# Kernel tuning notes

Measured on AMD Instinct MI355X. Metric: run time of the kernel, lower is better.

Reference implementation:

```python
import jax, jax.numpy as jnp
import numpy as np

N_EMBD = 384
HEAD_SIZE = 64
B, T = 512, 256


def setup_inputs() -> dict:
    key = jax.random.key(0)
    ks = jax.random.split(key, 7)
    s = 1.0 / np.sqrt(N_EMBD)  # torch Linear default init scale
    return {
        "x": jax.random.normal(ks[0], (B, T, N_EMBD), dtype=jnp.float32),
        "Wq": jax.random.uniform(ks[1], (N_EMBD, HEAD_SIZE), jnp.float32, -s, s),
        "bq": jax.random.uniform(ks[2], (HEAD_SIZE,), jnp.float32, -s, s),
        "Wk": jax.random.uniform(ks[3], (N_EMBD, HEAD_SIZE), jnp.float32, -s, s),
        "bk": jax.random.uniform(ks[4], (HEAD_SIZE,), jnp.float32, -s, s),
        "Wv": jax.random.uniform(ks[5], (N_EMBD, HEAD_SIZE), jnp.float32, -s, s),
        "bv": jax.random.uniform(ks[6], (HEAD_SIZE,), jnp.float32, -s, s),
    }


def reference(x, Wq, bq, Wk, bk, Wv, bv):
    # Single causal self-attention head (nanoGPT 'Head', eval mode: dropout = identity)
    q = x @ Wq + bq  # [B, T, H]
    k = x @ Wk + bk
    v = x @ Wv + bv
    Tq = x.shape[1]
    scale = x.shape[-1] ** -0.5  # NOTE: source scales by n_embd (C), not head_size
    wei = jnp.einsum("btd,bsd->bts", q, k) * scale  # [B, T, T]
    mask = jnp.tril(jnp.ones((Tq, Tq), dtype=bool))
    wei = jnp.where(mask, wei, -jnp.inf)
    wei = jax.nn.softmax(wei, axis=-1)
    return jnp.einsum("bts,bsd->btd", wei, v)  # [B, T, H]
```

## Files before the change

kernel.cpp:

```cpp
#include <hip/hip_runtime.h>
#include <hip/hip_bf16.h>


#define Bsz 512
#define Tt  256
#define Cc  384
#define Hh  64

typedef __attribute__((ext_vector_type(8))) short bf16x8;
typedef __attribute__((ext_vector_type(4))) float f32x4;

__device__ __forceinline__ unsigned short f2bf(float f) {
    unsigned int u = __float_as_uint(f);
    unsigned int r = (u + 0x7fffu + ((u >> 16) & 1u)) >> 16;
    return (unsigned short)r;
}
__device__ __forceinline__ float bf2f(unsigned short b) {
    return __uint_as_float(((unsigned int)b) << 16);
}
__device__ __forceinline__ bf16x8 pack8(float4 a, float4 b) {
    union { __hip_bfloat162 h2[4]; bf16x8 v; } u;
    u.h2[0] = __float22bfloat162_rn(float2{a.x, a.y});
    u.h2[1] = __float22bfloat162_rn(float2{a.z, a.w});
    u.h2[2] = __float22bfloat162_rn(float2{b.x, b.y});
    u.h2[3] = __float22bfloat162_rn(float2{b.z, b.w});
    return u.v;
}
__device__ __forceinline__ void gload_lds16(const void* g, void* l) {
    __builtin_amdgcn_global_load_lds(
        (const __attribute__((address_space(1))) unsigned int*)g,
        (__attribute__((address_space(3))) unsigned int*)l, 16, 0, 0);
}

__global__ __launch_bounds__(256) void prep_kernel(const float* __restrict__ Wq,
                                                   const float* __restrict__ Wk,
                                                   const float* __restrict__ Wv,
                                                   unsigned short* __restrict__ wtf) {
    int idx = blockIdx.x * 256 + threadIdx.x;
    if (idx >= 192 * 384) return;
    int j = idx & 7;
    int l = (idx >> 3) & 63;
    int t = idx >> 9;
    int kc = t / 12, nt = t - kc * 12;
    int n = nt * 16 + (l & 15);
    int k = kc * 32 + (l >> 4) * 8 + j;
    const float* W = (n < 64) ? Wq : ((n < 128) ? Wk : Wv);
    wtf[idx] = f2bf(W[k * 64 + (n & 63)]);
}

__global__ __launch_bounds__(512, 2) void fused_kernel(
        const float* __restrict__ x,
        const float* __restrict__ bq,
        const float* __restrict__ bk,
        const float* __restrict__ bv,
        const unsigned short* __restrict__ wtf,
        float* __restrict__ out) {
    __shared__ float xl[2][256 * 32];
    __shared__ unsigned short kl[16 * 128 * 8];
    __shared__ unsigned short vl[8 * 4 * 64 * 8];
    __shared__ unsigned short Pl[8 * 512];

    const int tid = threadIdx.x;
    const int w = tid >> 6, lane = tid & 63, quad = lane >> 4, cl = lane & 15;
    const int b = blockIdx.x;
    const int rb = b * 256;

    f32x4 acc[2][12];
#pragma unroll
    for (int rt = 0; rt < 2; ++rt)
#pragma unroll
        for (int nt = 0; nt < 12; ++nt) acc[rt][nt] = (f32x4){0.f, 0.f, 0.f, 0.f};

#pragma unroll
    for (int i = 0; i < 4; ++i) {
        int s = i * 512 + tid;
        int row = s >> 3, cp = s & 7;
        int c = cp ^ (row & 7);
        gload_lds16(x + (size_t)(rb + row) * Cc + c * 4, (char*)xl[0] + (size_t)s * 16);
    }

    for (int kc = 0; kc < 12; ++kc) {
        const int cur = kc & 1;
        bf16x8 bfr[12];
#pragma unroll
        for (int nt = 0; nt < 12; ++nt)
            bfr[nt] = *(const bf16x8*)&wtf[((size_t)(kc * 12 + nt) * 64 + lane) * 8];
        if (kc < 11) {
#pragma unroll
            for (int i = 0; i < 4; ++i) {
                int s = i * 512 + tid;
                int row = s >> 3, cp = s & 7;
                int c = cp ^ (row & 7);
                gload_lds16(x + (size_t)(rb + row) * Cc + (kc + 1) * 32 + c * 4,
                            (char*)xl[cur ^ 1] + (size_t)s * 16);
            }
            asm volatile("s_waitcnt vmcnt(4)" ::: "memory");
        } else {
            asm volatile("s_waitcnt vmcnt(0)" ::: "memory");
        }
        __builtin_amdgcn_s_barrier();

        bf16x8 a[2];
#pragma unroll
        for (int rt = 0; rt < 2; ++rt) {
            int R = w * 32 + rt * 16 + cl;
            float4 lo = *(const float4*)&xl[cur][R * 32 + (((2 * quad) ^ (R & 7)) * 4)];
            float4 hi = *(const float4*)&xl[cur][R * 32 + (((2 * quad + 1) ^ (R & 7)) * 4)];
            a[rt] = pack8(lo, hi);
        }
#pragma unroll
        for (int nt = 0; nt < 12; ++nt) {
            acc[0][nt] = __builtin_amdgcn_mfma_f32_16x16x32_bf16(a[0], bfr[nt], acc[0][nt], 0, 0, 0);
            acc[1][nt] = __builtin_amdgcn_mfma_f32_16x16x32_bf16(a[1], bfr[nt], acc[1][nt], 0, 0, 0);
        }
        __builtin_amdgcn_s_barrier();
    }

    unsigned short* qls = (unsigned short*)xl[0];
#pragma unroll
    for (int nt = 0; nt < 12; ++nt) {
        int col = nt * 16 + cl;
        if (nt < 4) {
            float bias = bq[col];
            int sh = col >> 5, qp = (col >> 3) & 3, j = col & 7;
#pragma unroll
            for (int rt = 0; rt < 2; ++rt) {
                int m0 = w * 32 + rt * 16 + quad * 4;
                int basei = (m0 >> 4) * 1024 + sh * 512 + qp * 128 + quad * 32 + j;
#pragma unroll
                for (int r = 0; r < 4; ++r)
                    qls[basei + r * 8] = f2bf(acc[rt][nt][r] + bias);
            }
        } else if (nt < 8) {
            int h = col & 63;
            float bias = bk[h];
            int sh = h >> 5, qp = (h >> 3) & 3, j = h & 7;
#pragma unroll
            for (int rt = 0; rt < 2; ++rt) {
                int m0 = w * 32 + rt * 16 + quad * 4;
                int basei = (m0 >> 4) * 1024 + sh * 512 + qp * 128 + quad * 32 + j;
#pragma unroll
                for (int r = 0; r < 4; ++r)
                    kl[basei + r * 8] = f2bf(acc[rt][nt][r] + bias);
            }
        } else {
            int h = col - 128;
            float bias = bv[h];
            int ht = h >> 4, clp = h & 15;
#pragma unroll
            for (int rt = 0; rt < 2; ++rt) {
                int m0 = w * 32 + rt * 16 + quad * 4;
                int ks2 = m0 >> 5, qp = (m0 >> 3) & 3, j0 = m0 & 7;
                unsigned long long pk =
                      (unsigned long long)f2bf(acc[rt][nt][0] + bias)
                    | ((unsigned long long)f2bf(acc[rt][nt][1] + bias) << 16)
                    | ((unsigned long long)f2bf(acc[rt][nt][2] + bias) << 32)
                    | ((unsigned long long)f2bf(acc[rt][nt][3] + bias) << 48);
                *(unsigned long long*)&vl[(ks2 * 4 + ht) * 512 + qp * 128 + clp * 8 + j0] = pk;
            }
        }
    }
    __syncthreads();

    const float SL2E = 0.07362224f;
    unsigned short* P = &Pl[w * 512];
#pragma unroll
    for (int ti = 0; ti < 2; ++ti) {
        const int W = ti ? (15 - w) : w;
        const int qrow0 = W * 16;
        bf16x8 aq0 = *(const bf16x8*)&qls[(W * 128 + lane) * 8];
        bf16x8 aq1 = *(const bf16x8*)&qls[(W * 128 + 64 + lane) * 8];

        f32x4 o[4];
#pragma unroll
        for (int ht = 0; ht < 4; ++ht) o[ht] = (f32x4){0.f, 0.f, 0.f, 0.f};
        float rs[4] = {0.f, 0.f, 0.f, 0.f};

        const int nsteps = (qrow0 >> 5) + 1;
        for (int st = 0; st < nsteps; ++st) {
#pragma unroll
            for (int half = 0; half < 2; ++half) {
                int ct = st * 2 + half;
                bf16x8 b0 = *(const bf16x8*)&kl[(ct * 128 + lane) * 8];
                bf16x8 b1 = *(const bf16x8*)&kl[(ct * 128 + 64 + lane) * 8];
                f32x4 sc = (f32x4){0.f, 0.f, 0.f, 0.f};
                sc = __builtin_amdgcn_mfma_f32_16x16x32_bf16(aq0, b0, sc, 0, 0, 0);
                sc = __builtin_amdgcn_mfma_f32_16x16x32_bf16(aq1, b1, sc, 0, 0, 0);
                int key = ct * 16 + cl;
#pragma unroll
                for (int r = 0; r < 4; ++r) {
                    int row = quad * 4 + r;
                    float p = (key <= qrow0 + row) ? exp2f(sc[r] * SL2E) : 0.f;
                    unsigned short pb = f2bf(p);
                    rs[r] += bf2f(pb);
                    int k32 = half * 16 + cl;
                    int chunk = (k32 >> 3) ^ quad;
                    P[row * 32 + chunk * 8 + (k32 & 7)] = pb;
                }
            }
            bf16x8 bvf[4];
#pragma unroll
            for (int ht = 0; ht < 4; ++ht)
                bvf[ht] = *(const bf16x8*)&vl[((st * 4 + ht) * 64 + lane) * 8];

            asm volatile("s_waitcnt lgkmcnt(0)" ::: "memory");
            bf16x8 ap = *(const bf16x8*)((const char*)P + cl * 64 + ((quad ^ (cl >> 2)) & 3) * 16);
#pragma unroll
            for (int ht = 0; ht < 4; ++ht)
                o[ht] = __builtin_amdgcn_mfma_f32_16x16x32_bf16(ap, bvf[ht], o[ht], 0, 0, 0);
        }

#pragma unroll
        for (int r = 0; r < 4; ++r) {
            float s = rs[r];
            s += __shfl_xor(s, 1);
            s += __shfl_xor(s, 2);
            s += __shfl_xor(s, 4);
            s += __shfl_xor(s, 8);
            float inv = 1.0f / s;
            int t = qrow0 + quad * 4 + r;
#pragma unroll
            for (int ht = 0; ht < 4; ++ht)
                out[((size_t)(b * Tt + t)) * Hh + ht * 16 + cl] = o[ht][r] * inv;
        }
    }
}

extern "C" void kernel_launch(void* const* d_in, const int* in_sizes, int n_in,
                              void* d_out, int out_size, void* d_ws, size_t ws_size,
                              hipStream_t stream) {
    const float* x  = (const float*)d_in[0];
    const float* Wq = (const float*)d_in[1];
    const float* bq = (const float*)d_in[2];
    const float* Wk = (const float*)d_in[3];
    const float* bk = (const float*)d_in[4];
    const float* Wv = (const float*)d_in[5];
    const float* bv = (const float*)d_in[6];
    float* out = (float*)d_out;

    unsigned short* wtf = (unsigned short*)d_ws;

    prep_kernel<<<288, 256, 0, stream>>>(Wq, Wk, Wv, wtf);
    fused_kernel<<<Bsz, 512, 0, stream>>>(x, bq, bk, bv, wtf, out);
}
```

Baseline: 320.8 us.

## Use 1024-thread blocks, stage weights in LDS, load x directly to registers

Doubles the block to 16 waves. The QKV projection is split so each wave computes 32 rows by 96 columns, and each attention wave handles one 16-row query tile instead of two. Weight fragments are now double-buffered in LDS through global_load_lds, shared by all waves. x is read straight from global memory into registers with a one-step prefetch, where before it was staged in LDS. The aim is more parallelism per block, fewer accumulator registers and fewer redundant global weight loads. The trade-off is that the causal work per wave becomes unbalanced, and launch_bounds(1024,4) may be unachievable given the LDS use.

```diff
diff --git a/kernel.cpp b/kernel.cpp
--- a/kernel.cpp
+++ b/kernel.cpp
@@ -18,12 +18,12 @@
 __device__ __forceinline__ float bf2f(unsigned short b) {
     return __uint_as_float(((unsigned int)b) << 16);
 }
-__device__ __forceinline__ bf16x8 pack8(float4 a, float4 b) {
+__device__ __forceinline__ bf16x8 pack8v(f32x4 a, f32x4 b) {
     union { __hip_bfloat162 h2[4]; bf16x8 v; } u;
-    u.h2[0] = __float22bfloat162_rn(float2{a.x, a.y});
-    u.h2[1] = __float22bfloat162_rn(float2{a.z, a.w});
-    u.h2[2] = __float22bfloat162_rn(float2{b.x, b.y});
-    u.h2[3] = __float22bfloat162_rn(float2{b.z, b.w});
+    u.h2[0] = __float22bfloat162_rn(float2{a[0], a[1]});
+    u.h2[1] = __float22bfloat162_rn(float2{a[2], a[3]});
+    u.h2[2] = __float22bfloat162_rn(float2{b[0], b[1]});
+    u.h2[3] = __float22bfloat162_rn(float2{b[2], b[3]});
     return u.v;
 }
 __device__ __forceinline__ void gload_lds16(const void* g, void* l) {
@@ -48,96 +48,96 @@
     wtf[idx] = f2bf(W[k * 64 + (n & 63)]);
 }
 
-__global__ __launch_bounds__(512, 2) void fused_kernel(
+__global__ __launch_bounds__(1024, 4) void fused_kernel(
         const float* __restrict__ x,
         const float* __restrict__ bq,
         const float* __restrict__ bk,
         const float* __restrict__ bv,
         const unsigned short* __restrict__ wtf,
         float* __restrict__ out) {
-    __shared__ float xl[2][256 * 32];
-    __shared__ unsigned short kl[16 * 128 * 8];
-    __shared__ unsigned short vl[8 * 4 * 64 * 8];
-    __shared__ unsigned short Pl[8 * 512];
+    __shared__ unsigned short kl[16384];
+    __shared__ unsigned short vl[16384];
+    __shared__ unsigned short ql[16384];
+    __shared__ unsigned short wtl[2][6144];
 
     const int tid = threadIdx.x;
     const int w = tid >> 6, lane = tid & 63, quad = lane >> 4, cl = lane & 15;
-    const int b = blockIdx.x;
-    const int rb = b * 256;
-
-    f32x4 acc[2][12];
+    const int wr = w & 7, wc = w >> 3;
+    const int rb = blockIdx.x * 256;
+
+    f32x4 acc[2][6];
 #pragma unroll
     for (int rt = 0; rt < 2; ++rt)
 #pragma unroll
-        for (int nt = 0; nt < 12; ++nt) acc[rt][nt] = (f32x4){0.f, 0.f, 0.f, 0.f};
-
-#pragma unroll
-    for (int i = 0; i < 4; ++i) {
-        int s = i * 512 + tid;
-        int row = s >> 3, cp = s & 7;
-        int c = cp ^ (row & 7);
-        gload_lds16(x + (size_t)(rb + row) * Cc + c * 4, (char*)xl[0] + (size_t)s * 16);
-    }
-
-    for (int kc = 0; kc < 12; ++kc) {
-        const int cur = kc & 1;
-        bf16x8 bfr[12];
-#pragma unroll
-        for (int nt = 0; nt < 12; ++nt)
-            bfr[nt] = *(const bf16x8*)&wtf[((size_t)(kc * 12 + nt) * 64 + lane) * 8];
-        if (kc < 11) {
-#pragma unroll
-            for (int i = 0; i < 4; ++i) {
-                int s = i * 512 + tid;
-                int row = s >> 3, cp = s & 7;
-                int c = cp ^ (row & 7);
-                gload_lds16(x + (size_t)(rb + row) * Cc + (kc + 1) * 32 + c * 4,
-                            (char*)xl[cur ^ 1] + (size_t)s * 16);
-            }
-            asm volatile("s_waitcnt vmcnt(4)" ::: "memory");
-        } else {
-            asm volatile("s_waitcnt vmcnt(0)" ::: "memory");
-        }
-        __builtin_amdgcn_s_barrier();
-
-        bf16x8 a[2];
-#pragma unroll
-        for (int rt = 0; rt < 2; ++rt) {
-            int R = w * 32 + rt * 16 + cl;
-            float4 lo = *(const float4*)&xl[cur][R * 32 + (((2 * quad) ^ (R & 7)) * 4)];
-            float4 hi = *(const float4*)&xl[cur][R * 32 + (((2 * quad + 1) ^ (R & 7)) * 4)];
-            a[rt] = pack8(lo, hi);
-        }
-#pragma unroll
-        for (int nt = 0; nt < 12; ++nt) {
-            acc[0][nt] = __builtin_amdgcn_mfma_f32_16x16x32_bf16(a[0], bfr[nt], acc[0][nt], 0, 0, 0);
-            acc[1][nt] = __builtin_amdgcn_mfma_f32_16x16x32_bf16(a[1], bfr[nt], acc[1][nt], 0, 0, 0);
-        }
-        __builtin_amdgcn_s_barrier();
-    }
-
-    unsigned short* qls = (unsigned short*)xl[0];
-#pragma unroll
-    for (int nt = 0; nt < 12; ++nt) {
-        int col = nt * 16 + cl;
-        if (nt < 4) {
+        for (int nt = 0; nt < 6; ++nt) acc[rt][nt] = (f32x4){0.f, 0.f, 0.f, 0.f};
+
+    const float* xp0 = x + (size_t)(rb + wr * 32 + cl) * Cc + quad * 8;
+    const float* xp1 = xp0 + (size_t)16 * Cc;
+    const bool dostage = tid < 768;
+    const unsigned short* wsrc = wtf + tid * 8;
+    unsigned short* wdst0 = &wtl[0][tid * 8];
+    unsigned short* wdst1 = &wtl[1][tid * 8];
+
+    if (dostage) gload_lds16(wsrc, wdst0);
+    f32x4 A0 = *(const f32x4*)(xp0);
+    f32x4 A1 = *(const f32x4*)(xp0 + 4);
+    f32x4 A2 = *(const f32x4*)(xp1);
+    f32x4 A3 = *(const f32x4*)(xp1 + 4);
+    f32x4 B0, B1, B2, B3;
+
+#define QKV_COMPUTE(BUF, X0, X1, X2, X3)                                             \
+    {                                                                                \
+        bf16x8 a0 = pack8v(X0, X1), a1 = pack8v(X2, X3);                             \
+        _Pragma("unroll")                                                            \
+        for (int nt = 0; nt < 6; ++nt) {                                             \
+            bf16x8 bfr = *(const bf16x8*)&wtl[BUF][((wc * 6 + nt) * 64 + lane) * 8]; \
+            acc[0][nt] = __builtin_amdgcn_mfma_f32_16x16x32_bf16(a0, bfr, acc[0][nt], 0, 0, 0); \
+            acc[1][nt] = __builtin_amdgcn_mfma_f32_16x16x32_bf16(a1, bfr, acc[1][nt], 0, 0, 0); \
+        }                                                                            \
+    }
+
+    for (int t = 0; t < 6; ++t) {
+        const int kc = 2 * t;
+        __syncthreads();
+        if (dostage) gload_lds16(wsrc + (size_t)(kc + 1) * 6144, wdst1);
+        B0 = *(const f32x4*)(xp0 + (kc + 1) * 32);
+        B1 = *(const f32x4*)(xp0 + (kc + 1) * 32 + 4);
+        B2 = *(const f32x4*)(xp1 + (kc + 1) * 32);
+        B3 = *(const f32x4*)(xp1 + (kc + 1) * 32 + 4);
+        QKV_COMPUTE(0, A0, A1, A2, A3)
+        __syncthreads();
+        if (t < 5) {
+            if (dostage) gload_lds16(wsrc + (size_t)(kc + 2) * 6144, wdst0);
+            A0 = *(const f32x4*)(xp0 + (kc + 2) * 32);
+            A1 = *(const f32x4*)(xp0 + (kc + 2) * 32 + 4);
+            A2 = *(const f32x4*)(xp1 + (kc + 2) * 32);
+            A3 = *(const f32x4*)(xp1 + (kc + 2) * 32 + 4);
+        }
+        QKV_COMPUTE(1, B0, B1, B2, B3)
+    }
+
+#pragma unroll
+    for (int nt = 0; nt < 6; ++nt) {
+        const int colbase = wc * 96 + nt * 16;
+        const int col = colbase + cl;
+        if (colbase < 64) {
             float bias = bq[col];
             int sh = col >> 5, qp = (col >> 3) & 3, j = col & 7;
 #pragma unroll
             for (int rt = 0; rt < 2; ++rt) {
-                int m0 = w * 32 + rt * 16 + quad * 4;
+                int m0 = wr * 32 + rt * 16 + quad * 4;
                 int basei = (m0 >> 4) * 1024 + sh * 512 + qp * 128 + quad * 32 + j;
 #pragma unroll
                 for (int r = 0; r < 4; ++r)
-                    qls[basei + r * 8] = f2bf(acc[rt][nt][r] + bias);
-            }
-        } else if (nt < 8) {
-            int h = col & 63;
+                    ql[basei + r * 8] = f2bf(acc[rt][nt][r] + bias);
+            }
+        } else if (colbase < 128) {
+            int h = col - 64;
             float bias = bk[h];
             int sh = h >> 5, qp = (h >> 3) & 3, j = h & 7;
 #pragma unroll
             for (int rt = 0; rt < 2; ++rt) {
-                int m0 = w * 32 + rt * 16 + quad * 4;
+                int m0 = wr * 32 + rt * 16 + quad * 4;
                 int basei = (m0 >> 4) * 1024 + sh * 512 + qp * 128 + quad * 32 + j;
 #pragma unroll
                 for (int r = 0; r < 4; ++r)
@@ -146,30 +146,29 @@
         } else {
             int h = col - 128;
             float bias = bv[h];
-            int ht = h >> 4, clp = h & 15;
+            int ht = h >> 4;
 #pragma unroll
             for (int rt = 0; rt < 2; ++rt) {
-                int m0 = w * 32 + rt * 16 + quad * 4;
+                int m0 = wr * 32 + rt * 16 + quad * 4;
                 int ks2 = m0 >> 5, qp = (m0 >> 3) & 3, j0 = m0 & 7;
                 unsigned long long pk =
                       (unsigned long long)f2bf(acc[rt][nt][0] + bias)
                     | ((unsigned long long)f2bf(acc[rt][nt][1] + bias) << 16)
                     | ((unsigned long long)f2bf(acc[rt][nt][2] + bias) << 32)
                     | ((unsigned long long)f2bf(acc[rt][nt][3] + bias) << 48);
-                *(unsigned long long*)&vl[(ks2 * 4 + ht) * 512 + qp * 128 + clp * 8 + j0] = pk;
+                *(unsigned long long*)&vl[(ks2 * 4 + ht) * 512 + qp * 128 + cl * 8 + j0] = pk;
             }
         }
     }
     __syncthreads();
 
     const float SL2E = 0.07362224f;
-    unsigned short* P = &Pl[w * 512];
-#pragma unroll
-    for (int ti = 0; ti < 2; ++ti) {
-        const int W = ti ? (15 - w) : w;
+    unsigned short* P = &wtl[0][0] + w * 512;
+    {
+        const int W = w;
         const int qrow0 = W * 16;
-        bf16x8 aq0 = *(const bf16x8*)&qls[(W * 128 + lane) * 8];
-        bf16x8 aq1 = *(const bf16x8*)&qls[(W * 128 + 64 + lane) * 8];
+        bf16x8 aq0 = *(const bf16x8*)&ql[(W * 128 + lane) * 8];
+        bf16x8 aq1 = *(const bf16x8*)&ql[(W * 128 + 64 + lane) * 8];
 
         f32x4 o[4];
 #pragma unroll
@@ -221,7 +220,7 @@
             int t = qrow0 + quad * 4 + r;
 #pragma unroll
             for (int ht = 0; ht < 4; ++ht)
-                out[((size_t)(b * Tt + t)) * Hh + ht * 16 + cl] = o[ht][r] * inv;
+                out[((size_t)(blockIdx.x * Tt + t)) * Hh + ht * 16 + cl] = o[ht][r] * inv;
         }
     }
 }
@@ -241,5 +240,5 @@
     unsigned short* wtf = (unsigned short*)d_ws;
 
     prep_kernel<<<288, 256, 0, stream>>>(Wq, Wk, Wv, wtf);
-    fused_kernel<<<Bsz, 512, 0, stream>>>(x, bq, bk, bv, wtf, out);
-}
+    fused_kernel<<<Bsz, 1024, 0, stream>>>(x, bq, bk, bv, wtf, out);
+}
```

New measurement: 323.1 us. No clear change (+0.7%).
